# Kernel optimization log

Measured on AMD Instinct MI355X. Metric: run time of the kernel, lower is better.

Reference implementation:

```python
import jax, jax.numpy as jnp
import numpy as np

H = 1024      # hidden_size
V = 50257     # output_size (vocab)
L = 18        # max_length


def setup_inputs() -> dict:
    key = jax.random.key(0)
    ks = jax.random.split(key, 16)
    s = 0.02
    return {
        "input_ids": jax.random.randint(ks[0], (1,), 0, V),
        "hidden": jax.random.normal(ks[1], (1, 1, H), jnp.float32),
        "encoder_outputs": jax.random.normal(ks[2], (L, H), jnp.float32),
        "emb": jax.random.normal(ks[3], (V, H), jnp.float32) * s,
        "attn_W": jax.random.normal(ks[4], (L, 2 * H), jnp.float32) * s,
        "attn_b": jax.random.normal(ks[5], (L,), jnp.float32) * s,
        "comb_W": jax.random.normal(ks[6], (H, 2 * H), jnp.float32) * s,
        "comb_b": jax.random.normal(ks[7], (H,), jnp.float32) * s,
        "gru_Wih": jax.random.normal(ks[8], (3 * H, H), jnp.float32) * s,
        "gru_Whh": jax.random.normal(ks[9], (3 * H, H), jnp.float32) * s,
        "gru_bih": jax.random.normal(ks[10], (3 * H,), jnp.float32) * s,
        "gru_bhh": jax.random.normal(ks[11], (3 * H,), jnp.float32) * s,
        "out_W": jax.random.normal(ks[12], (V, H), jnp.float32) * s,
        "out_b": jax.random.normal(ks[13], (V,), jnp.float32) * s,
    }


def reference(input_ids, hidden, encoder_outputs, emb, attn_W, attn_b,
              comb_W, comb_b, gru_Wih, gru_Whh, gru_bih, gru_bhh,
              out_W, out_b):
    # embedding lookup -> [1, H]; dropout in eval mode = identity
    embedded = emb[input_ids[0]][None, :]
    h = hidden[0]  # [1, H]
    # additive attention over fixed-length encoder outputs
    attn_weights = jax.nn.softmax(
        jnp.concatenate([embedded, h], axis=1) @ attn_W.T + attn_b, axis=1)  # [1, L]
    attn_applied = attn_weights @ encoder_outputs  # [1, H]
    # combine + relu
    x = jnp.concatenate([embedded, attn_applied], axis=1) @ comb_W.T + comb_b
    x = jax.nn.relu(x)  # [1, H] -> GRU input
    # single-step GRU (PyTorch gate ordering r, z, n)
    gi = x @ gru_Wih.T + gru_bih  # [1, 3H]
    gh = h @ gru_Whh.T + gru_bhh  # [1, 3H]
    i_r, i_z, i_n = jnp.split(gi, 3, axis=1)
    h_r, h_z, h_n = jnp.split(gh, 3, axis=1)
    r = jax.nn.sigmoid(i_r + h_r)
    z = jax.nn.sigmoid(i_z + h_z)
    n = jnp.tanh(i_n + r * h_n)
    h_new = (1.0 - z) * n + z * h  # [1, H]
    # output log-probs over vocab
    logits = h_new @ out_W.T + out_b  # [1, V]
    log_probs = jax.nn.log_softmax(logits, axis=1)
    return (log_probs, h_new[None], attn_weights)
```

## Files before the change

kernel.cpp:

```cpp
#include <hip/hip_runtime.h>
#include <math.h>

#define H 1024
#define V 50257
#define L 18

#define WS_CAT   0
#define WS_X     2080
#define WS_GH    3104
#define WS_HNEW  6176
#define WS_PAIRS 7200
#define NBLK4    2048

__device__ __forceinline__ float waveReduceSum(float v) {
#pragma unroll
    for (int off = 32; off > 0; off >>= 1) v += __shfl_xor(v, off);
    return v;
}

__global__ __launch_bounds__(256) void k1_attn(
    const int* __restrict__ ids, const float* __restrict__ hidden,
    const float* __restrict__ enc, const float* __restrict__ emb,
    const float* __restrict__ attn_W, const float* __restrict__ attn_b,
    float* __restrict__ ws, float* __restrict__ out)
{
    __shared__ float s_scores[32];
    __shared__ float s_w[L];
    const int t = threadIdx.x;
    const int wave = t >> 6, lane = t & 63;
    const int id = ids[0];
    const float* erow = emb + (size_t)id * H;

    for (int i = t; i < H; i += 256) ws[WS_CAT + i] = erow[i];

    const float4* e4 = (const float4*)erow;
    const float4* h4 = (const float4*)hidden;
    float4 ereg[4], hreg[4];
#pragma unroll
    for (int k = 0; k < 4; ++k) { ereg[k] = e4[lane + k * 64]; hreg[k] = h4[lane + k * 64]; }

    for (int l = wave; l < L; l += 4) {
        const float4* r4 = (const float4*)(attn_W + (size_t)l * 2 * H);
        float acc = 0.f;
#pragma unroll
        for (int k = 0; k < 4; ++k) {
            float4 a = r4[lane + k * 64];
            acc += a.x * ereg[k].x + a.y * ereg[k].y + a.z * ereg[k].z + a.w * ereg[k].w;
        }
#pragma unroll
        for (int k = 0; k < 4; ++k) {
            float4 a = r4[256 + lane + k * 64];
            acc += a.x * hreg[k].x + a.y * hreg[k].y + a.z * hreg[k].z + a.w * hreg[k].w;
        }
        acc = waveReduceSum(acc);
        if (lane == 0) s_scores[l] = acc + attn_b[l];
    }
    __syncthreads();

    if (wave == 0) {
        float v = (lane < L) ? s_scores[lane] : -INFINITY;
        float m = v;
#pragma unroll
        for (int off = 32; off > 0; off >>= 1) m = fmaxf(m, __shfl_xor(m, off));
        float e = (lane < L) ? expf(v - m) : 0.f;
        float s = waveReduceSum(e);
        float w = e / s;
        if (lane < L) {
            s_w[lane] = w;
            out[(size_t)V + H + lane] = w;
        }
    }
    __syncthreads();

    for (int i = t; i < H; i += 256) {
        float acc = 0.f;
#pragma unroll
        for (int l = 0; l < L; ++l) acc += s_w[l] * enc[l * H + i];
        ws[WS_CAT + H + i] = acc;
    }
}

__global__ __launch_bounds__(256) void k2_comb_gh(
    const float* __restrict__ hidden,
    const float* __restrict__ comb_W, const float* __restrict__ comb_b,
    const float* __restrict__ Whh, const float* __restrict__ bhh,
    float* __restrict__ ws)
{
    const int t = threadIdx.x;
    const int wave = t >> 6, lane = t & 63;
    const int r = blockIdx.x * 4 + wave;

    if (r < H) {
        const float4* c4 = (const float4*)(ws + WS_CAT);
        float4 creg[8];
#pragma unroll
        for (int k = 0; k < 8; ++k) creg[k] = c4[lane + k * 64];
        const float4* r4 = (const float4*)(comb_W + (size_t)r * 2 * H);
        float acc = 0.f;
#pragma unroll
        for (int k = 0; k < 8; ++k) {
            float4 a = r4[lane + k * 64];
            acc += a.x * creg[k].x + a.y * creg[k].y + a.z * creg[k].z + a.w * creg[k].w;
        }
        acc = waveReduceSum(acc);
        if (lane == 0) ws[WS_X + r] = fmaxf(acc + comb_b[r], 0.f);
    } else {
        const int r2 = r - H;
        const float4* h4 = (const float4*)hidden;
        float4 hreg[4];
#pragma unroll
        for (int k = 0; k < 4; ++k) hreg[k] = h4[lane + k * 64];
        const float4* r4 = (const float4*)(Whh + (size_t)r2 * H);
        float acc = 0.f;
#pragma unroll
        for (int k = 0; k < 4; ++k) {
            float4 a = r4[lane + k * 64];
            acc += a.x * hreg[k].x + a.y * hreg[k].y + a.z * hreg[k].z + a.w * hreg[k].w;
        }
        acc = waveReduceSum(acc);
        if (lane == 0) ws[WS_GH + r2] = acc + bhh[r2];
    }
}

__global__ __launch_bounds__(256) void k3_gru(
    const float* __restrict__ hidden,
    const float* __restrict__ Wih, const float* __restrict__ bih,
    float* __restrict__ ws, float* __restrict__ out)
{
    const int t = threadIdx.x;
    const int wave = t >> 6, lane = t & 63;
    const int j = blockIdx.x * 4 + wave;

    const float4* x4 = (const float4*)(ws + WS_X);
    float4 xreg[4];
#pragma unroll
    for (int k = 0; k < 4; ++k) xreg[k] = x4[lane + k * 64];

    float d[3];
#pragma unroll
    for (int g = 0; g < 3; ++g) {
        const float4* r4 = (const float4*)(Wih + (size_t)(g * H + j) * H);
        float acc = 0.f;
#pragma unroll
        for (int k = 0; k < 4; ++k) {
            float4 a = r4[lane + k * 64];
            acc += a.x * xreg[k].x + a.y * xreg[k].y + a.z * xreg[k].z + a.w * xreg[k].w;
        }
        d[g] = waveReduceSum(acc);
    }
    if (lane == 0) {
        float i_r = d[0] + bih[j];
        float i_z = d[1] + bih[H + j];
        float i_n = d[2] + bih[2 * H + j];
        float h_r = ws[WS_GH + j];
        float h_z = ws[WS_GH + H + j];
        float h_n = ws[WS_GH + 2 * H + j];
        float hj  = hidden[j];
        float rg = 1.f / (1.f + expf(-(i_r + h_r)));
        float zg = 1.f / (1.f + expf(-(i_z + h_z)));
        float ng = tanhf(i_n + rg * h_n);
        float hn = (1.f - zg) * ng + zg * hj;
        ws[WS_HNEW + j] = hn;
        out[(size_t)V + j] = hn;
    }
}

__global__ __launch_bounds__(256) void k4_logits(
    const float* __restrict__ out_W, const float* __restrict__ out_b,
    float* __restrict__ ws, float* __restrict__ out)
{
    __shared__ float s_m[4], s_s[4];
    const int t = threadIdx.x;
    const int wave = t >> 6, lane = t & 63;
    const int gw = blockIdx.x * 4 + wave;
    const int NW = NBLK4 * 4;

    const float4* h4 = (const float4*)(ws + WS_HNEW);
    float4 hreg[4];
#pragma unroll
    for (int k = 0; k < 4; ++k) hreg[k] = h4[lane + k * 64];

    float m = -INFINITY, s = 0.f;
    for (int v = gw * 2; v < V; v += NW * 2) {
        const int v1 = v + 1;
        const float4* r4a = (const float4*)(out_W + (size_t)v * H);
        float acc0 = 0.f, acc1 = 0.f;
        if (v1 < V) {
            const float4* r4b = (const float4*)(out_W + (size_t)v1 * H);
#pragma unroll
            for (int k = 0; k < 4; ++k) {
                float4 a = r4a[lane + k * 64];
                float4 b = r4b[lane + k * 64];
                acc0 += a.x * hreg[k].x + a.y * hreg[k].y + a.z * hreg[k].z + a.w * hreg[k].w;
                acc1 += b.x * hreg[k].x + b.y * hreg[k].y + b.z * hreg[k].z + b.w * hreg[k].w;
            }
        } else {
#pragma unroll
            for (int k = 0; k < 4; ++k) {
                float4 a = r4a[lane + k * 64];
                acc0 += a.x * hreg[k].x + a.y * hreg[k].y + a.z * hreg[k].z + a.w * hreg[k].w;
            }
        }
        acc0 = waveReduceSum(acc0);
        acc1 = waveReduceSum(acc1);
        float logit0 = acc0 + out_b[v];
        if (lane == 0) out[v] = logit0;
        float mn = fmaxf(m, logit0);
        s = s * expf(m - mn) + expf(logit0 - mn);
        m = mn;
        if (v1 < V) {
            float logit1 = acc1 + out_b[v1];
            if (lane == 0) out[v1] = logit1;
            mn = fmaxf(m, logit1);
            s = s * expf(m - mn) + expf(logit1 - mn);
            m = mn;
        }
    }
    if (lane == 0) { s_m[wave] = m; s_s[wave] = s; }
    __syncthreads();
    if (t == 0) {
        float M = s_m[0], S = s_s[0];
#pragma unroll
        for (int w = 1; w < 4; ++w) {
            float m2 = s_m[w], s2 = s_s[w];
            float Mn = fmaxf(M, m2);
            S = S * expf(M - Mn) + s2 * expf(m2 - Mn);
            M = Mn;
        }
        ws[WS_PAIRS + blockIdx.x * 2]     = M;
        ws[WS_PAIRS + blockIdx.x * 2 + 1] = S;
    }
}

__global__ __launch_bounds__(256) void k5_lse_sub(
    float* __restrict__ ws, float* __restrict__ out)
{
    __shared__ float s_m[256], s_s[256];
    const int t = threadIdx.x;
    float M = -INFINITY, S = 0.f;
    for (int i = t; i < NBLK4; i += 256) {
        float m2 = ws[WS_PAIRS + i * 2], s2 = ws[WS_PAIRS + i * 2 + 1];
        float Mn = fmaxf(M, m2);
        S = S * expf(M - Mn) + s2 * expf(m2 - Mn);
        M = Mn;
    }
    s_m[t] = M; s_s[t] = S;
    __syncthreads();
    for (int off = 128; off > 0; off >>= 1) {
        if (t < off) {
            float m2 = s_m[t + off], s2 = s_s[t + off];
            float Mn = fmaxf(s_m[t], m2);
            s_s[t] = s_s[t] * expf(s_m[t] - Mn) + s2 * expf(m2 - Mn);
            s_m[t] = Mn;
        }
        __syncthreads();
    }
    const float lse = s_m[0] + logf(s_s[0]);
    const int n = gridDim.x * 256;
    for (int v = blockIdx.x * 256 + t; v < V; v += n) out[v] -= lse;
}

extern "C" void kernel_launch(void* const* d_in, const int* in_sizes, int n_in,
                              void* d_out, int out_size, void* d_ws, size_t ws_size,
                              hipStream_t stream) {
    const int*   ids    = (const int*)  d_in[0];
    const float* hidden = (const float*)d_in[1];
    const float* enc    = (const float*)d_in[2];
    const float* emb    = (const float*)d_in[3];
    const float* attn_W = (const float*)d_in[4];
    const float* attn_b = (const float*)d_in[5];
    const float* comb_W = (const float*)d_in[6];
    const float* comb_b = (const float*)d_in[7];
    const float* Wih    = (const float*)d_in[8];
    const float* Whh    = (const float*)d_in[9];
    const float* bih    = (const float*)d_in[10];
    const float* bhh    = (const float*)d_in[11];
    const float* out_W  = (const float*)d_in[12];
    const float* out_b  = (const float*)d_in[13];
    float* out = (float*)d_out;
    float* ws  = (float*)d_ws;

    hipLaunchKernelGGL(k1_attn,    dim3(1),     dim3(256), 0, stream,
                       ids, hidden, enc, emb, attn_W, attn_b, ws, out);
    hipLaunchKernelGGL(k2_comb_gh, dim3(1024),  dim3(256), 0, stream,
                       hidden, comb_W, comb_b, Whh, bhh, ws);
    hipLaunchKernelGGL(k3_gru,     dim3(256),   dim3(256), 0, stream,
                       hidden, Wih, bih, ws, out);
    hipLaunchKernelGGL(k4_logits,  dim3(NBLK4), dim3(256), 0, stream,
                       out_W, out_b, ws, out);
    hipLaunchKernelGGL(k5_lse_sub, dim3(128),   dim3(256), 0, stream,
                       ws, out);
}
```

Before: 437.5 us.

## Fuse GRU and logits stages into one persistent kernel with grid barriers

Merges the comb/Whh, GRU, logits and log-softmax stages into a single kernel of 512 blocks that sync through software grid barriers built on atomics in the workspace, and widens the attention kernel to 1024 threads. The aim is to remove several kernel launch gaps and the serialization between small dependent stages. The cost is barrier spin time, and correctness relies on all 512 blocks being co-resident (launch bounds request 2 blocks per CU). The barrier counters are reset by the preceding kernel on each call.

```diff
diff --git a/kernel.cpp b/kernel.cpp
--- a/kernel.cpp
+++ b/kernel.cpp
@@ -4,13 +4,15 @@
 #define H 1024
 #define V 50257
 #define L 18
+#define NBLK 512
+#define NWAVE 2048
 
 #define WS_CAT   0
 #define WS_X     2080
 #define WS_GH    3104
 #define WS_HNEW  6176
 #define WS_PAIRS 7200
-#define NBLK4    2048
+#define WS_BAR   11296
 
 __device__ __forceinline__ float waveReduceSum(float v) {
 #pragma unroll
@@ -18,7 +20,24 @@
     return v;
 }
 
-__global__ __launch_bounds__(256) void k1_attn(
+__device__ __forceinline__ void gbar(unsigned* bar, int id, unsigned nblk) {
+    __syncthreads();
+    if (threadIdx.x == 0) {
+        unsigned* cnt  = bar + 2 * id;
+        unsigned* flag = bar + 2 * id + 1;
+        __threadfence();
+        if (atomicAdd(cnt, 1u) == nblk - 1u) {
+            __hip_atomic_store(flag, 1u, __ATOMIC_RELEASE, __HIP_MEMORY_SCOPE_AGENT);
+        } else {
+            while (__hip_atomic_load(flag, __ATOMIC_ACQUIRE, __HIP_MEMORY_SCOPE_AGENT) == 0u)
+                __builtin_amdgcn_s_sleep(8);
+        }
+        __threadfence();
+    }
+    __syncthreads();
+}
+
+__global__ __launch_bounds__(1024) void k_front(
     const int* __restrict__ ids, const float* __restrict__ hidden,
     const float* __restrict__ enc, const float* __restrict__ emb,
     const float* __restrict__ attn_W, const float* __restrict__ attn_b,
@@ -28,10 +47,13 @@
     __shared__ float s_w[L];
     const int t = threadIdx.x;
     const int wave = t >> 6, lane = t & 63;
+
+    if (t < 8) ((unsigned*)(ws + WS_BAR))[t] = 0u;
+
     const int id = ids[0];
     const float* erow = emb + (size_t)id * H;
 
-    for (int i = t; i < H; i += 256) ws[WS_CAT + i] = erow[i];
+    ws[WS_CAT + t] = erow[t];
 
     const float4* e4 = (const float4*)erow;
     const float4* h4 = (const float4*)hidden;
@@ -39,7 +61,7 @@
 #pragma unroll
     for (int k = 0; k < 4; ++k) { ereg[k] = e4[lane + k * 64]; hreg[k] = h4[lane + k * 64]; }
 
-    for (int l = wave; l < L; l += 4) {
+    for (int l = wave; l < L; l += 16) {
         const float4* r4 = (const float4*)(attn_W + (size_t)l * 2 * H);
         float acc = 0.f;
 #pragma unroll
@@ -72,116 +94,115 @@
     }
     __syncthreads();
 
-    for (int i = t; i < H; i += 256) {
-        float acc = 0.f;
-#pragma unroll
-        for (int l = 0; l < L; ++l) acc += s_w[l] * enc[l * H + i];
-        ws[WS_CAT + H + i] = acc;
-    }
-}
-
-__global__ __launch_bounds__(256) void k2_comb_gh(
+    {
+        float acc = 0.f;
+#pragma unroll
+        for (int l = 0; l < L; ++l) acc += s_w[l] * enc[l * H + t];
+        ws[WS_CAT + H + t] = acc;
+    }
+}
+
+__global__ __launch_bounds__(256, 2) void k_big(
     const float* __restrict__ hidden,
     const float* __restrict__ comb_W, const float* __restrict__ comb_b,
     const float* __restrict__ Whh, const float* __restrict__ bhh,
-    float* __restrict__ ws)
-{
-    const int t = threadIdx.x;
-    const int wave = t >> 6, lane = t & 63;
-    const int r = blockIdx.x * 4 + wave;
-
-    if (r < H) {
-        const float4* c4 = (const float4*)(ws + WS_CAT);
-        float4 creg[8];
-#pragma unroll
-        for (int k = 0; k < 8; ++k) creg[k] = c4[lane + k * 64];
-        const float4* r4 = (const float4*)(comb_W + (size_t)r * 2 * H);
-        float acc = 0.f;
-#pragma unroll
-        for (int k = 0; k < 8; ++k) {
-            float4 a = r4[lane + k * 64];
-            acc += a.x * creg[k].x + a.y * creg[k].y + a.z * creg[k].z + a.w * creg[k].w;
-        }
-        acc = waveReduceSum(acc);
-        if (lane == 0) ws[WS_X + r] = fmaxf(acc + comb_b[r], 0.f);
-    } else {
-        const int r2 = r - H;
-        const float4* h4 = (const float4*)hidden;
-        float4 hreg[4];
-#pragma unroll
-        for (int k = 0; k < 4; ++k) hreg[k] = h4[lane + k * 64];
-        const float4* r4 = (const float4*)(Whh + (size_t)r2 * H);
-        float acc = 0.f;
-#pragma unroll
-        for (int k = 0; k < 4; ++k) {
-            float4 a = r4[lane + k * 64];
-            acc += a.x * hreg[k].x + a.y * hreg[k].y + a.z * hreg[k].z + a.w * hreg[k].w;
-        }
-        acc = waveReduceSum(acc);
-        if (lane == 0) ws[WS_GH + r2] = acc + bhh[r2];
-    }
-}
-
-__global__ __launch_bounds__(256) void k3_gru(
-    const float* __restrict__ hidden,
     const float* __restrict__ Wih, const float* __restrict__ bih,
-    float* __restrict__ ws, float* __restrict__ out)
-{
-    const int t = threadIdx.x;
-    const int wave = t >> 6, lane = t & 63;
-    const int j = blockIdx.x * 4 + wave;
-
-    const float4* x4 = (const float4*)(ws + WS_X);
-    float4 xreg[4];
-#pragma unroll
-    for (int k = 0; k < 4; ++k) xreg[k] = x4[lane + k * 64];
-
-    float d[3];
-#pragma unroll
-    for (int g = 0; g < 3; ++g) {
-        const float4* r4 = (const float4*)(Wih + (size_t)(g * H + j) * H);
-        float acc = 0.f;
-#pragma unroll
-        for (int k = 0; k < 4; ++k) {
-            float4 a = r4[lane + k * 64];
-            acc += a.x * xreg[k].x + a.y * xreg[k].y + a.z * xreg[k].z + a.w * xreg[k].w;
-        }
-        d[g] = waveReduceSum(acc);
-    }
-    if (lane == 0) {
-        float i_r = d[0] + bih[j];
-        float i_z = d[1] + bih[H + j];
-        float i_n = d[2] + bih[2 * H + j];
-        float h_r = ws[WS_GH + j];
-        float h_z = ws[WS_GH + H + j];
-        float h_n = ws[WS_GH + 2 * H + j];
-        float hj  = hidden[j];
-        float rg = 1.f / (1.f + expf(-(i_r + h_r)));
-        float zg = 1.f / (1.f + expf(-(i_z + h_z)));
-        float ng = tanhf(i_n + rg * h_n);
-        float hn = (1.f - zg) * ng + zg * hj;
-        ws[WS_HNEW + j] = hn;
-        out[(size_t)V + j] = hn;
-    }
-}
-
-__global__ __launch_bounds__(256) void k4_logits(
     const float* __restrict__ out_W, const float* __restrict__ out_b,
     float* __restrict__ ws, float* __restrict__ out)
 {
-    __shared__ float s_m[4], s_s[4];
+    __shared__ float s_a[256], s_b[256];
+    unsigned* bar = (unsigned*)(ws + WS_BAR);
     const int t = threadIdx.x;
-    const int wave = t >> 6, lane = t & 63;
-    const int gw = blockIdx.x * 4 + wave;
-    const int NW = NBLK4 * 4;
-
-    const float4* h4 = (const float4*)(ws + WS_HNEW);
+    const int wid = t >> 6, lane = t & 63;
+    const int W = blockIdx.x * 4 + wid;
+
+    const float4* h4 = (const float4*)hidden;
     float4 hreg[4];
 #pragma unroll
     for (int k = 0; k < 4; ++k) hreg[k] = h4[lane + k * 64];
 
+    if (W < 1024) {
+        const float4* c4 = (const float4*)(ws + WS_CAT);
+        float4 creg[8];
+#pragma unroll
+        for (int k = 0; k < 8; ++k) creg[k] = c4[lane + k * 64];
+        const float4* r4 = (const float4*)(comb_W + (size_t)W * 2 * H);
+        float acc = 0.f;
+#pragma unroll
+        for (int k = 0; k < 8; ++k) {
+            float4 a = r4[lane + k * 64];
+            acc += a.x * creg[k].x + a.y * creg[k].y + a.z * creg[k].z + a.w * creg[k].w;
+        }
+        acc = waveReduceSum(acc);
+        if (lane == 0) ws[WS_X + W] = fmaxf(acc + comb_b[W], 0.f);
+    } else {
+        const int r2 = W - 1024;
+        const float4* r4 = (const float4*)(Whh + (size_t)r2 * H);
+        float acc = 0.f;
+#pragma unroll
+        for (int k = 0; k < 4; ++k) {
+            float4 a = r4[lane + k * 64];
+            acc += a.x * hreg[k].x + a.y * hreg[k].y + a.z * hreg[k].z + a.w * hreg[k].w;
+        }
+        acc = waveReduceSum(acc);
+        if (lane == 0) ws[WS_GH + r2] = acc + bhh[r2];
+    }
+    {
+        const int r3 = W + 1024;
+        const float4* r4 = (const float4*)(Whh + (size_t)r3 * H);
+        float acc = 0.f;
+#pragma unroll
+        for (int k = 0; k < 4; ++k) {
+            float4 a = r4[lane + k * 64];
+            acc += a.x * hreg[k].x + a.y * hreg[k].y + a.z * hreg[k].z + a.w * hreg[k].w;
+        }
+        acc = waveReduceSum(acc);
+        if (lane == 0) ws[WS_GH + r3] = acc + bhh[r3];
+    }
+    gbar(bar, 0, NBLK);
+
+    if (W < H) {
+        const float4* x4 = (const float4*)(ws + WS_X);
+        float4 xreg[4];
+#pragma unroll
+        for (int k = 0; k < 4; ++k) xreg[k] = x4[lane + k * 64];
+        float d[3];
+#pragma unroll
+        for (int g = 0; g < 3; ++g) {
+            const float4* r4 = (const float4*)(Wih + (size_t)(g * H + W) * H);
+            float acc = 0.f;
+#pragma unroll
+            for (int k = 0; k < 4; ++k) {
+                float4 a = r4[lane + k * 64];
+                acc += a.x * xreg[k].x + a.y * xreg[k].y + a.z * xreg[k].z + a.w * xreg[k].w;
+            }
+            d[g] = waveReduceSum(acc);
+        }
+        if (lane == 0) {
+            float i_r = d[0] + bih[W];
+            float i_z = d[1] + bih[H + W];
+            float i_n = d[2] + bih[2 * H + W];
+            float h_r = ws[WS_GH + W];
+            float h_z = ws[WS_GH + H + W];
+            float h_n = ws[WS_GH + 2 * H + W];
+            float hj  = hidden[W];
+            float rg = 1.f / (1.f + expf(-(i_r + h_r)));
+            float zg = 1.f / (1.f + expf(-(i_z + h_z)));
+            float ng = tanhf(i_n + rg * h_n);
+            float hn = (1.f - zg) * ng + zg * hj;
+            ws[WS_HNEW + W] = hn;
+            out[(size_t)V + W] = hn;
+        }
+    }
+    gbar(bar, 1, NBLK);
+
+    const float4* n4 = (const float4*)(ws + WS_HNEW);
+    float4 nreg[4];
+#pragma unroll
+    for (int k = 0; k < 4; ++k) nreg[k] = n4[lane + k * 64];
+
     float m = -INFINITY, s = 0.f;
-    for (int v = gw * 2; v < V; v += NW * 2) {
+    for (int v = W * 2; v < V; v += NWAVE * 2) {
         const int v1 = v + 1;
         const float4* r4a = (const float4*)(out_W + (size_t)v * H);
         float acc0 = 0.f, acc1 = 0.f;
@@ -191,14 +212,14 @@
             for (int k = 0; k < 4; ++k) {
                 float4 a = r4a[lane + k * 64];
                 float4 b = r4b[lane + k * 64];
-                acc0 += a.x * hreg[k].x + a.y * hreg[k].y + a.z * hreg[k].z + a.w * hreg[k].w;
-                acc1 += b.x * hreg[k].x + b.y * hreg[k].y + b.z * hreg[k].z + b.w * hreg[k].w;
+                acc0 += a.x * nreg[k].x + a.y * nreg[k].y + a.z * nreg[k].z + a.w * nreg[k].w;
+                acc1 += b.x * nreg[k].x + b.y * nreg[k].y + b.z * nreg[k].z + b.w * nreg[k].w;
             }
         } else {
 #pragma unroll
             for (int k = 0; k < 4; ++k) {
                 float4 a = r4a[lane + k * 64];
-                acc0 += a.x * hreg[k].x + a.y * hreg[k].y + a.z * hreg[k].z + a.w * hreg[k].w;
+                acc0 += a.x * nreg[k].x + a.y * nreg[k].y + a.z * nreg[k].z + a.w * nreg[k].w;
             }
         }
         acc0 = waveReduceSum(acc0);
@@ -216,48 +237,32 @@
             m = mn;
         }
     }
-    if (lane == 0) { s_m[wave] = m; s_s[wave] = s; }
-    __syncthreads();
-    if (t == 0) {
-        float M = s_m[0], S = s_s[0];
-#pragma unroll
-        for (int w = 1; w < 4; ++w) {
-            float m2 = s_m[w], s2 = s_s[w];
-            float Mn = fmaxf(M, m2);
-            S = S * expf(M - Mn) + s2 * expf(m2 - Mn);
-            M = Mn;
-        }
-        ws[WS_PAIRS + blockIdx.x * 2]     = M;
-        ws[WS_PAIRS + blockIdx.x * 2 + 1] = S;
-    }
-}
-
-__global__ __launch_bounds__(256) void k5_lse_sub(
-    float* __restrict__ ws, float* __restrict__ out)
-{
-    __shared__ float s_m[256], s_s[256];
-    const int t = threadIdx.x;
+    if (lane == 0) {
+        ws[WS_PAIRS + W * 2]     = m;
+        ws[WS_PAIRS + W * 2 + 1] = s;
+    }
+    gbar(bar, 2, NBLK);
+
     float M = -INFINITY, S = 0.f;
-    for (int i = t; i < NBLK4; i += 256) {
+    for (int i = t; i < NWAVE; i += 256) {
         float m2 = ws[WS_PAIRS + i * 2], s2 = ws[WS_PAIRS + i * 2 + 1];
         float Mn = fmaxf(M, m2);
         S = S * expf(M - Mn) + s2 * expf(m2 - Mn);
         M = Mn;
     }
-    s_m[t] = M; s_s[t] = S;
+    s_a[t] = M; s_b[t] = S;
     __syncthreads();
     for (int off = 128; off > 0; off >>= 1) {
         if (t < off) {
-            float m2 = s_m[t + off], s2 = s_s[t + off];
-            float Mn = fmaxf(s_m[t], m2);
-            s_s[t] = s_s[t] * expf(s_m[t] - Mn) + s2 * expf(m2 - Mn);
-            s_m[t] = Mn;
+            float m2 = s_a[t + off], s2 = s_b[t + off];
+            float Mn = fmaxf(s_a[t], m2);
+            s_b[t] = s_b[t] * expf(s_a[t] - Mn) + s2 * expf(m2 - Mn);
+            s_a[t] = Mn;
         }
         __syncthreads();
     }
-    const float lse = s_m[0] + logf(s_s[0]);
-    const int n = gridDim.x * 256;
-    for (int v = blockIdx.x * 256 + t; v < V; v += n) out[v] -= lse;
+    const float lse = s_a[0] + logf(s_b[0]);
+    for (int v = blockIdx.x * 256 + t; v < V; v += NBLK * 256) out[v] -= lse;
 }
 
 extern "C" void kernel_launch(void* const* d_in, const int* in_sizes, int n_in,
@@ -280,14 +285,9 @@
     float* out = (float*)d_out;
     float* ws  = (float*)d_ws;
 
-    hipLaunchKernelGGL(k1_attn,    dim3(1),     dim3(256), 0, stream,
+    hipLaunchKernelGGL(k_front, dim3(1),    dim3(1024), 0, stream,
                        ids, hidden, enc, emb, attn_W, attn_b, ws, out);
-    hipLaunchKernelGGL(k2_comb_gh, dim3(1024),  dim3(256), 0, stream,
-                       hidden, comb_W, comb_b, Whh, bhh, ws);
-    hipLaunchKernelGGL(k3_gru,     dim3(256),   dim3(256), 0, stream,
-                       hidden, Wih, bih, ws, out);
-    hipLaunchKernelGGL(k4_logits,  dim3(NBLK4), dim3(256), 0, stream,
+    hipLaunchKernelGGL(k_big,   dim3(NBLK), dim3(256),  0, stream,
+                       hidden, comb_W, comb_b, Whh, bhh, Wih, bih,
                        out_W, out_b, ws, out);
-    hipLaunchKernelGGL(k5_lse_sub, dim3(128),   dim3(256), 0, stream,
-                       ws, out);
-}
+}
```

New measurement: 598.9 us. 36.9% more time.
